# Kernel tuning notes

Hardware: AMD Instinct MI355X
Metric: run time of the kernel (lower is better)

## Reference

```python
import jax, jax.numpy as jnp
import numpy as np

B, T, D, L = 64, 512, 768, 5  # x batch is 2*B (MRC pairing), label_dim = L


def setup_inputs() -> dict:
    key = jax.random.key(0)
    k1, k2, k3, k4, k5 = jax.random.split(key, 5)
    x = jax.random.normal(k1, (2 * B, T, D), jnp.float32)
    label = jax.random.randint(k2, (B, T), 0, L - 1)            # values 0..L-2 so label+1 < L
    seqlen = jax.random.randint(k3, (B,), 2, T + 1)             # >=2 avoids degenerate CRF paths
    W = jax.random.normal(k4, (D, L), jnp.float32) * 0.02       # Dense kernel (TruncatedNormal 0.02)
    b = jnp.zeros((L,), jnp.float32)
    transitions = jax.random.normal(k5, (L, L), jnp.float32) * 0.1  # glorot-ish
    return {"x": x, "label": label, "seqlen": seqlen, "W": W, "b": b, "transitions": transitions}


def crf_log_norm(logits, seqlen, trans):
    # logits: [N, T, L]; forward algorithm with alphas frozen past seqlen
    ts = jnp.arange(1, logits.shape[1])

    def step(alpha, inp):
        x, t = inp  # x: [N, L]
        new = x + jax.nn.logsumexp(alpha[:, :, None] + trans[None], axis=1)
        return jnp.where((t < seqlen)[:, None], new, alpha), None

    alpha, _ = jax.lax.scan(step, logits[:, 0], (jnp.swapaxes(logits[:, 1:], 0, 1), ts))
    return jax.nn.logsumexp(alpha, axis=-1)


def crf_sequence_score(logits, tags, seqlen, trans):
    N, Tn, Ln = logits.shape
    t_idx = jnp.arange(Tn)
    mask = (t_idx[None, :] < seqlen[:, None]).astype(logits.dtype)          # [N, T]
    unary = jnp.take_along_axis(logits, tags[:, :, None], axis=2)[:, :, 0]  # [N, T]
    unary = jnp.sum(unary * mask, axis=1)
    binary = trans[tags[:, :-1], tags[:, 1:]]                               # [N, T-1]
    mask2 = (t_idx[None, 1:] < seqlen[:, None]).astype(logits.dtype)
    binary = jnp.sum(binary * mask2, axis=1)
    return unary + binary


def crf_decode(logits, trans, seqlen):
    # Viterbi: forward max + backpointers (identity past seqlen), then backtrack
    N, Tn, Ln = logits.shape
    ts = jnp.arange(1, Tn)
    ident = jnp.broadcast_to(jnp.arange(Ln)[None, :], (N, Ln))

    def fwd(state, inp):
        x, t = inp
        scores = state[:, :, None] + trans[None]   # [N, L_prev, L_cur]
        bp = jnp.argmax(scores, axis=1)            # [N, L]
        new = x + jnp.max(scores, axis=1)
        keep = (t < seqlen)[:, None]
        return jnp.where(keep, new, state), jnp.where(keep, bp, ident)

    last, bps = jax.lax.scan(fwd, logits[:, 0], (jnp.swapaxes(logits[:, 1:], 0, 1), ts))
    last_tag = jnp.argmax(last, axis=-1)           # [N]

    def bwd(tag, bp):
        prev = jnp.take_along_axis(bp, tag[:, None], axis=1)[:, 0]
        return prev, tag

    first_tag, rev_tags = jax.lax.scan(bwd, last_tag, bps, reverse=True)
    return jnp.concatenate([first_tag[:, None], jnp.swapaxes(rev_tags, 0, 1)], axis=1)  # [N, T]


def reference(x, label, seqlen, W, b, transitions):
    logits = x @ W + b                                   # [2B, T, L]
    label1 = jnp.where(label > 0, jnp.ones_like(label), label)
    label2 = jnp.where(label > 0, label + 1, label)
    label_r = jnp.concatenate([label1, label2], axis=0)  # [2B, T]
    seqlen_r = jnp.tile(seqlen, 2)                       # [2B]
    ll = crf_sequence_score(logits, label_r, seqlen_r, transitions) - crf_log_norm(logits, seqlen_r, transitions)
    loss = jnp.mean(-ll)
    vit = crf_decode(logits, transitions, seqlen_r)      # [2B, T]
    v1, v2 = jnp.split(vit, 2, axis=0)
    viterbi = jnp.where((v1 == 0) | (v2 == 0), jnp.zeros_like(v1), v2 - 1)
    mask = (jnp.arange(x.shape[1])[None, :] < seqlen[:, None]).astype(jnp.float32)
    acc = jnp.sum((viterbi == label).astype(jnp.float32) * mask) / jnp.sum(seqlen.astype(jnp.float32))
    return viterbi, loss, acc
```

## Files before the change

### kernel.cpp

```cpp
#include <hip/hip_runtime.h>

#define BB 64
#define TT 512
#define DD 768
#define LL 5
#define NSEQ 128
#define NTOK 65536
#define NEG_INF (-1e30f)
#define IDENT_W 0x4688u

__device__ __forceinline__ float wave_sum_dpp(float v) {
    int t;
    t = __builtin_amdgcn_update_dpp(0, __float_as_int(v), 0x111, 0xf, 0xf, false);
    v += __int_as_float(t);
    t = __builtin_amdgcn_update_dpp(0, __float_as_int(v), 0x112, 0xf, 0xf, false);
    v += __int_as_float(t);
    t = __builtin_amdgcn_update_dpp(0, __float_as_int(v), 0x114, 0xf, 0xf, false);
    v += __int_as_float(t);
    t = __builtin_amdgcn_update_dpp(0, __float_as_int(v), 0x118, 0xf, 0xf, false);
    v += __int_as_float(t);
    t = __builtin_amdgcn_update_dpp(0, __float_as_int(v), 0x142, 0xa, 0xf, false);
    v += __int_as_float(t);
    t = __builtin_amdgcn_update_dpp(0, __float_as_int(v), 0x143, 0xc, 0xf, false);
    v += __int_as_float(t);
    return v;
}

__global__ __launch_bounds__(256) void k_logits(const float* __restrict__ x,
                                                const float* __restrict__ W,
                                                const float* __restrict__ bias,
                                                const int* __restrict__ seqlen,
                                                float* __restrict__ logits) {
    const int lane = threadIdx.x & 63;
    const int w    = blockIdx.x * 4 + (threadIdx.x >> 6);
    const int n    = w & 127;
    const int slot = w >> 7;
    const int sl   = seqlen[n & (BB - 1)];
    if (slot >= sl) return;

    float wreg[3][4][LL];
    {
        const float4* W4 = reinterpret_cast<const float4*>(W);
#pragma unroll
        for (int p = 0; p < 3; ++p) {
            const int base4 = p * 320 + lane * 5;
#pragma unroll
            for (int j = 0; j < 5; ++j) {
                const float4 v = W4[base4 + j];
                wreg[p][(j * 4 + 0) / 5][(j * 4 + 0) % 5] = v.x;
                wreg[p][(j * 4 + 1) / 5][(j * 4 + 1) % 5] = v.y;
                wreg[p][(j * 4 + 2) / 5][(j * 4 + 2) % 5] = v.z;
                wreg[p][(j * 4 + 3) / 5][(j * 4 + 3) % 5] = v.w;
            }
        }
    }
    float breg[LL];
#pragma unroll
    for (int l = 0; l < LL; ++l) breg[l] = bias[l];

    const float* xb = x + (size_t)n * TT * DD;
    float* lb = logits + (size_t)n * TT * LL;

#pragma unroll
    for (int pp = 0; pp < 4; ++pp) {
        const int tA = slot + 128 * pp;
        if (tA >= sl) break;
        const int tB = tA + 64;
        const bool aB = (tB < sl);

        const float4* xpA = reinterpret_cast<const float4*>(xb + (size_t)tA * DD);
        const float4* xpB = reinterpret_cast<const float4*>(xb + (size_t)tB * DD);
        float4 vA[3], vB[3];
#pragma unroll
        for (int p = 0; p < 3; ++p) vA[p] = xpA[p * 64 + lane];
        if (aB) {
#pragma unroll
            for (int p = 0; p < 3; ++p) vB[p] = xpB[p * 64 + lane];
        }

        float accA[LL] = {0.f, 0.f, 0.f, 0.f, 0.f};
        float accB[LL] = {0.f, 0.f, 0.f, 0.f, 0.f};
#pragma unroll
        for (int p = 0; p < 3; ++p) {
#pragma unroll
            for (int l = 0; l < LL; ++l) {
                accA[l] += vA[p].x * wreg[p][0][l] + vA[p].y * wreg[p][1][l] +
                           vA[p].z * wreg[p][2][l] + vA[p].w * wreg[p][3][l];
            }
        }
        if (aB) {
#pragma unroll
            for (int p = 0; p < 3; ++p) {
#pragma unroll
                for (int l = 0; l < LL; ++l) {
                    accB[l] += vB[p].x * wreg[p][0][l] + vB[p].y * wreg[p][1][l] +
                               vB[p].z * wreg[p][2][l] + vB[p].w * wreg[p][3][l];
                }
            }
        }

#pragma unroll
        for (int l = 0; l < LL; ++l) accA[l] = wave_sum_dpp(accA[l]);
        if (aB) {
#pragma unroll
            for (int l = 0; l < LL; ++l) accB[l] = wave_sum_dpp(accB[l]);
        }

        if (lane == 63) {
#pragma unroll
            for (int l = 0; l < LL; ++l) lb[(size_t)tA * LL + l] = accA[l] + breg[l];
            if (aB) {
#pragma unroll
                for (int l = 0; l < LL; ++l) lb[(size_t)tB * LL + l] = accB[l] + breg[l];
            }
        }
    }
}

__global__ __launch_bounds__(512) void k_scan4(const float* __restrict__ logits,
                                               const int* __restrict__ label,
                                               const int* __restrict__ seqlen,
                                               const float* __restrict__ trans,
                                               float* __restrict__ out,
                                               float* __restrict__ losspart,
                                               int* __restrict__ okpart) {
    __shared__ float s_lg[2][TT * LL + 8];
    __shared__ float s_P[1600];
    __shared__ float s_Q[800];
    __shared__ float s_A[2][33 * 5];
    __shared__ float s_tr[25];
    __shared__ float s_etr[25];
    __shared__ unsigned s_mapw[2][32];
    __shared__ int s_B[2][33];
    __shared__ int s_tags[2][TT];
    __shared__ float s_ws[8];
    __shared__ int s_wok[8];

    const int tid = threadIdx.x;
    const int bid = blockIdx.x;

    if (bid < 128) {
        const int n  = bid;
        const int sl = seqlen[n & (BB - 1)];
        const float* lg = logits + (size_t)n * TT * LL;
        if (tid < 25) { const float tv = trans[tid]; s_tr[tid] = tv; s_etr[tid] = __expf(tv); }
        const int lim = sl * LL;
        for (int i = tid; i < lim; i += 512) s_lg[0][i] = lg[i];
        __syncthreads();

        {
            const bool sec = (n >= BB);
            const int* lab = label + (n & (BB - 1)) * TT;
            const int t = tid;
            float sc = 0.f;
            if (t < sl) {
                const int lv = lab[t];
                const int tg = (lv > 0) ? (sec ? lv + 1 : 1) : 0;
                sc = s_lg[0][t * 5 + tg];
                if (t >= 1) {
                    const int lp = lab[t - 1];
                    const int tp = (lp > 0) ? (sec ? lp + 1 : 1) : 0;
                    sc += s_tr[tp * 5 + tg];
                }
            }
#pragma unroll
            for (int off = 32; off > 0; off >>= 1) sc += __shfl_xor(sc, off, 64);
            if ((tid & 63) == 0) s_ws[tid >> 6] = sc;
        }

        if (tid < 320) {
            const int c = tid / 5, r = tid - 5 * c;
            float p[5];
#pragma unroll
            for (int j = 0; j < 5; ++j) p[j] = (j == r) ? 0.f : NEG_INF;
#pragma unroll
            for (int i = 0; i < 8; ++i) {
                const int t = c * 8 + 1 + i;
                const bool act = t < sl;
                const float m = fmaxf(fmaxf(fmaxf(p[0], p[1]), fmaxf(p[2], p[3])), p[4]);
                float e[5];
#pragma unroll
                for (int k = 0; k < 5; ++k) e[k] = __expf(p[k] - m);
                float nv[5];
#pragma unroll
                for (int j = 0; j < 5; ++j) {
                    float s = e[0] * s_etr[j];
#pragma unroll
                    for (int k = 1; k < 5; ++k) s += e[k] * s_etr[k * 5 + j];
                    nv[j] = m + __logf(s) + s_lg[0][t * 5 + j];
                }
#pragma unroll
                for (int j = 0; j < 5; ++j) p[j] = act ? nv[j] : p[j];
            }
#pragma unroll
            for (int j = 0; j < 5; ++j) s_P[c * 25 + r * 5 + j] = p[j];
        }
        __syncthreads();

#pragma unroll
        for (int lev = 0; lev < 6; ++lev) {
            const int np = 32 >> lev;
            const float* inb = (lev & 1) ? s_Q : s_P;
            float* outb      = (lev & 1) ? s_P : s_Q;
            for (int task = tid; task < np * 25; task += 512) {
                const int pm = task / 25;
                const int e  = task - pm * 25;
                const int r  = e / 5, j = e - 5 * r;
                const float* A  = inb + (2 * pm) * 25;
                const float* Bm = inb + (2 * pm + 1) * 25;
                float v[5];
#pragma unroll
                for (int k = 0; k < 5; ++k) v[k] = A[r * 5 + k] + Bm[k * 5 + j];
                float m = fmaxf(fmaxf(fmaxf(v[0], v[1]), fmaxf(v[2], v[3])), v[4]);
                float ssum = 0.f;
#pragma unroll
                for (int k = 0; k < 5; ++k) ssum += __expf(v[k] - m);
                outb[pm * 25 + e] = m + __logf(ssum);
            }
            __syncthreads();
        }

        if (tid == 0) {
            float b[5];
#pragma unroll
            for (int j = 0; j < 5; ++j) {
                float v[5];
#pragma unroll
                for (int k = 0; k < 5; ++k) v[k] = s_lg[0][k] + s_P[k * 5 + j];
                float m = fmaxf(fmaxf(fmaxf(v[0], v[1]), fmaxf(v[2], v[3])), v[4]);
                float ssum = 0.f;
#pragma unroll
                for (int k = 0; k < 5; ++k) ssum += __expf(v[k] - m);
                b[j] = m + __logf(ssum);
            }
            float m = fmaxf(fmaxf(fmaxf(b[0], b[1]), fmaxf(b[2], b[3])), b[4]);
            float ssum = 0.f;
#pragma unroll
            for (int j = 0; j < 5; ++j) ssum += __expf(b[j] - m);
            const float ln = m + __logf(ssum);
            float sc = 0.f;
#pragma unroll
            for (int wv = 0; wv < 8; ++wv) sc += s_ws[wv];
            losspart[n] = ln - sc;
        }
    } else {
        const int bb = bid - 128;
        const int sl = seqlen[bb];
        const float* lgA = logits + (size_t)bb * TT * LL;
        const float* lgB = logits + (size_t)(bb + BB) * TT * LL;

        if (tid < 25) s_tr[tid] = trans[tid];
        {
            const int lim = sl * LL;
            for (int i = tid; i < lim; i += 512) { s_lg[0][i] = lgA[i]; s_lg[1][i] = lgB[i]; }
        }
        __syncthreads();

        const int sid = tid / 160;
        const int rem = tid - sid * 160;
        const int cc  = rem / 5;
        const int rr  = rem - cc * 5;

        if (tid < 320) {
            float p[5];
#pragma unroll
            for (int j = 0; j < 5; ++j) p[j] = (j == rr) ? 0.f : NEG_INF;
#pragma unroll
            for (int i = 0; i < 16; ++i) {
                const int t = cc * 16 + 1 + i;
                const bool act = t < sl;
                float nv[5];
#pragma unroll
                for (int j = 0; j < 5; ++j) {
                    float b = p[0] + s_tr[j];
#pragma unroll
                    for (int k = 1; k < 5; ++k) b = fmaxf(b, p[k] + s_tr[k * 5 + j]);
                    nv[j] = b + s_lg[sid][t * 5 + j];
                }
#pragma unroll
                for (int j = 0; j < 5; ++j) p[j] = act ? nv[j] : p[j];
            }
#pragma unroll
            for (int j = 0; j < 5; ++j) s_P[sid * 800 + cc * 25 + rr * 5 + j] = p[j];
        }
        __syncthreads();

#pragma unroll
        for (int st = 1; st < 32; st <<= 1) {
            float Ar[5], Bm[25];
            const bool doit = (tid < 320) && (cc >= st);
            if (doit) {
#pragma unroll
                for (int k = 0; k < 5; ++k) Ar[k] = s_P[sid * 800 + (cc - st) * 25 + rr * 5 + k];
#pragma unroll
                for (int e = 0; e < 25; ++e) Bm[e] = s_P[sid * 800 + cc * 25 + e];
            }
            __syncthreads();
            if (doit) {
#pragma unroll
                for (int j = 0; j < 5; ++j) {
                    float b = Ar[0] + Bm[j];
#pragma unroll
                    for (int k = 1; k < 5; ++k) b = fmaxf(b, Ar[k] + Bm[k * 5 + j]);
                    s_P[sid * 800 + cc * 25 + rr * 5 + j] = b;
                }
            }
            __syncthreads();
        }

        if (tid < 320) {
            float b = s_lg[sid][0] + s_P[sid * 800 + cc * 25 + rr];
#pragma unroll
            for (int k = 1; k < 5; ++k)
                b = fmaxf(b, s_lg[sid][k] + s_P[sid * 800 + cc * 25 + k * 5 + rr]);
            s_A[sid][(cc + 1) * 5 + rr] = b;
        } else if (tid < 330) {
            const int i2 = tid - 320;
            const int s = i2 / 5, j = i2 - 5 * s;
            s_A[s][j] = s_lg[s][j];
        }
        __syncthreads();

        unsigned bpw[16];
        const int vs = tid >> 5, vc = tid & 31;
        if (tid < 64) {
            float a[5];
#pragma unroll
            for (int j = 0; j < 5; ++j) a[j] = s_A[vs][vc * 5 + j];
#pragma unroll
            for (int i = 0; i < 16; ++i) {
                const int t = vc * 16 + 1 + i;
                const bool act = t < sl;
                float nv[5]; int gi[5];
#pragma unroll
                for (int j = 0; j < 5; ++j) {
                    float b = a[0] + s_tr[j]; int g = 0;
#pragma unroll
                    for (int k = 1; k < 5; ++k) {
                        const float cn = a[k] + s_tr[k * 5 + j];
                        if (cn > b) { b = cn; g = k; }
                    }
                    nv[j] = b + s_lg[vs][t * 5 + j]; gi[j] = g;
                }
                const unsigned wv = (unsigned)gi[0] | ((unsigned)gi[1] << 3) |
                                    ((unsigned)gi[2] << 6) | ((unsigned)gi[3] << 9) |
                                    ((unsigned)gi[4] << 12);
                bpw[i] = act ? wv : IDENT_W;
#pragma unroll
                for (int j = 0; j < 5; ++j) a[j] = act ? nv[j] : a[j];
            }
            int m[5] = {0, 1, 2, 3, 4};
#pragma unroll
            for (int i = 15; i >= 0; --i) {
                const unsigned wv = bpw[i];
#pragma unroll
                for (int j = 0; j < 5; ++j) m[j] = (int)((wv >> (3 * m[j])) & 7u);
            }
            s_mapw[vs][vc] = (unsigned)m[0] | ((unsigned)m[1] << 3) | ((unsigned)m[2] << 6) |
                             ((unsigned)m[3] << 9) | ((unsigned)m[4] << 12);
        }
        __syncthreads();

        if (tid < 2) {
            const int s = tid;
            float b = s_A[s][32 * 5 + 0]; int lt = 0;
#pragma unroll
            for (int j = 1; j < 5; ++j) {
                const float cn = s_A[s][32 * 5 + j];
                if (cn > b) { b = cn; lt = j; }
            }
            unsigned wv[32];
#pragma unroll
            for (int c = 0; c < 32; ++c) wv[c] = s_mapw[s][c];
            int bc = lt; s_B[s][32] = lt;
#pragma unroll
            for (int c = 31; c >= 0; --c) { bc = (int)((wv[c] >> (3 * bc)) & 7u); s_B[s][c] = bc; }
        }
        __syncthreads();

        if (tid < 64) {
            int cur = s_B[vs][vc + 1];
#pragma unroll
            for (int i = 15; i >= 0; --i) {
                cur = (int)((bpw[i] >> (3 * cur)) & 7u);
                s_tags[vs][vc * 16 + i] = cur;
            }
        }
        __syncthreads();

        {
            const int t = tid;
            const int* lab = label + bb * TT;
            const int t1 = s_tags[0][t];
            const int t2 = s_tags[1][t];
            const int vit = (t1 == 0 || t2 == 0) ? 0 : (t2 - 1);
            out[bb * TT + t] = (float)vit;
            int ok = ((vit == lab[t]) && (t < sl)) ? 1 : 0;
#pragma unroll
            for (int off = 32; off > 0; off >>= 1) ok += __shfl_xor(ok, off, 64);
            if ((tid & 63) == 0) s_wok[tid >> 6] = ok;
        }
        __syncthreads();
        if (tid == 0) {
            int ok = 0;
#pragma unroll
            for (int wv = 0; wv < 8; ++wv) ok += s_wok[wv];
            okpart[bb] = ok;
        }
    }
}

__global__ __launch_bounds__(128) void k_final(const float* __restrict__ losspart,
                                               const int* __restrict__ okpart,
                                               const int* __restrict__ seqlen,
                                               float* __restrict__ out) {
    __shared__ float sf[2];
    __shared__ int s1[2], s2[2];
    const int tid = threadIdx.x;
    float f = losspart[tid];
    int ok = (tid < BB) ? okpart[tid] : 0;
    int sl = (tid < BB) ? seqlen[tid] : 0;
#pragma unroll
    for (int off = 32; off > 0; off >>= 1) {
        f  += __shfl_xor(f, off, 64);
        ok += __shfl_xor(ok, off, 64);
        sl += __shfl_xor(sl, off, 64);
    }
    if ((tid & 63) == 0) { sf[tid >> 6] = f; s1[tid >> 6] = ok; s2[tid >> 6] = sl; }
    __syncthreads();
    if (tid == 0) {
        out[BB * TT]     = (sf[0] + sf[1]) / (float)NSEQ;
        out[BB * TT + 1] = (float)(s1[0] + s1[1]) / (float)(s2[0] + s2[1]);
    }
}

extern "C" void kernel_launch(void* const* d_in, const int* in_sizes, int n_in,
                              void* d_out, int out_size, void* d_ws, size_t ws_size,
                              hipStream_t stream) {
    const float* x      = (const float*)d_in[0];
    const int*   label  = (const int*)d_in[1];
    const int*   seqlen = (const int*)d_in[2];
    const float* W      = (const float*)d_in[3];
    const float* bias   = (const float*)d_in[4];
    const float* trans  = (const float*)d_in[5];
    float* out = (float*)d_out;
    char*  ws  = (char*)d_ws;

    float* ws_logits   = (float*)(ws);
    float* ws_losspart = (float*)(ws + 1310720);
    int*   ws_okpart   = (int*)(ws + 1311232);

    hipLaunchKernelGGL(k_logits, dim3(2048), dim3(256), 0, stream,
                       x, W, bias, seqlen, ws_logits);
    hipLaunchKernelGGL(k_scan4, dim3(192), dim3(512), 0, stream,
                       ws_logits, label, seqlen, trans, out, ws_losspart, ws_okpart);
    hipLaunchKernelGGL(k_final, dim3(1), dim3(128), 0, stream,
                       ws_losspart, ws_okpart, seqlen, out);
}
```

Before: 39.55 us.

## Compact valid tokens via seqlen prefix sum for balanced logits GEMV

The logits kernel now builds a per-block prefix sum of sequence lengths and enumerates only valid tokens. Each wave takes tokens in a grid-stride loop and finds its sequence with a binary search. This replaces the fixed (sequence, slot) wave mapping, whose per-wave work was uneven across sequences of different lengths. In exchange, every block repeats the 128-element scan with several barriers, and each wave now processes one token per iteration instead of two, which reduces memory-level parallelism per wave.

```diff
diff --git a/kernel.cpp b/kernel.cpp
--- a/kernel.cpp
+++ b/kernel.cpp
@@ -31,12 +31,27 @@
                                                 const float* __restrict__ bias,
                                                 const int* __restrict__ seqlen,
                                                 float* __restrict__ logits) {
-    const int lane = threadIdx.x & 63;
-    const int w    = blockIdx.x * 4 + (threadIdx.x >> 6);
-    const int n    = w & 127;
-    const int slot = w >> 7;
-    const int sl   = seqlen[n & (BB - 1)];
-    if (slot >= sl) return;
+    __shared__ int sP[129];
+    __shared__ int tmp[128];
+    const int tid = threadIdx.x;
+
+    if (tid < 128) tmp[tid] = seqlen[tid & (BB - 1)];
+    __syncthreads();
+#pragma unroll
+    for (int off = 1; off < 128; off <<= 1) {
+        int v = 0;
+        if (tid < 128 && tid >= off) v = tmp[tid - off];
+        __syncthreads();
+        if (tid < 128) tmp[tid] += v;
+        __syncthreads();
+    }
+    if (tid < 128) sP[tid + 1] = tmp[tid];
+    if (tid == 0) sP[0] = 0;
+    __syncthreads();
+    const int A = sP[128];
+
+    const int lane = tid & 63;
+    const int wid  = blockIdx.x * 4 + (tid >> 6);
 
     float wreg[3][4][LL];
     {
@@ -58,61 +73,39 @@
 #pragma unroll
     for (int l = 0; l < LL; ++l) breg[l] = bias[l];
 
-    const float* xb = x + (size_t)n * TT * DD;
-    float* lb = logits + (size_t)n * TT * LL;
-
-#pragma unroll
-    for (int pp = 0; pp < 4; ++pp) {
-        const int tA = slot + 128 * pp;
-        if (tA >= sl) break;
-        const int tB = tA + 64;
-        const bool aB = (tB < sl);
-
-        const float4* xpA = reinterpret_cast<const float4*>(xb + (size_t)tA * DD);
-        const float4* xpB = reinterpret_cast<const float4*>(xb + (size_t)tB * DD);
-        float4 vA[3], vB[3];
-#pragma unroll
-        for (int p = 0; p < 3; ++p) vA[p] = xpA[p * 64 + lane];
-        if (aB) {
-#pragma unroll
-            for (int p = 0; p < 3; ++p) vB[p] = xpB[p * 64 + lane];
-        }
-
-        float accA[LL] = {0.f, 0.f, 0.f, 0.f, 0.f};
-        float accB[LL] = {0.f, 0.f, 0.f, 0.f, 0.f};
-#pragma unroll
-        for (int p = 0; p < 3; ++p) {
-#pragma unroll
-            for (int l = 0; l < LL; ++l) {
-                accA[l] += vA[p].x * wreg[p][0][l] + vA[p].y * wreg[p][1][l] +
-                           vA[p].z * wreg[p][2][l] + vA[p].w * wreg[p][3][l];
-            }
-        }
-        if (aB) {
-#pragma unroll
-            for (int p = 0; p < 3; ++p) {
-#pragma unroll
-                for (int l = 0; l < LL; ++l) {
-                    accB[l] += vB[p].x * wreg[p][0][l] + vB[p].y * wreg[p][1][l] +
-                               vB[p].z * wreg[p][2][l] + vB[p].w * wreg[p][3][l];
-                }
-            }
-        }
-
-#pragma unroll
-        for (int l = 0; l < LL; ++l) accA[l] = wave_sum_dpp(accA[l]);
-        if (aB) {
-#pragma unroll
-            for (int l = 0; l < LL; ++l) accB[l] = wave_sum_dpp(accB[l]);
-        }
+    for (int g = wid; g < A; g += 8192) {
+        int lo = 0, hi = 128;
+#pragma unroll
+        for (int s = 0; s < 7; ++s) {
+            const int mid = (lo + hi) >> 1;
+            if (sP[mid] <= g) lo = mid; else hi = mid;
+        }
+        const int n = lo;
+        const int t = g - sP[lo];
+        const size_t tok = (size_t)n * TT + t;
+
+        const float4* xp = reinterpret_cast<const float4*>(x + tok * DD);
+        float4 v0 = xp[lane];
+        float4 v1 = xp[64 + lane];
+        float4 v2 = xp[128 + lane];
+
+        float acc[LL];
+#pragma unroll
+        for (int l = 0; l < LL; ++l) {
+            acc[l] = v0.x * wreg[0][0][l] + v0.y * wreg[0][1][l] +
+                     v0.z * wreg[0][2][l] + v0.w * wreg[0][3][l] +
+                     v1.x * wreg[1][0][l] + v1.y * wreg[1][1][l] +
+                     v1.z * wreg[1][2][l] + v1.w * wreg[1][3][l] +
+                     v2.x * wreg[2][0][l] + v2.y * wreg[2][1][l] +
+                     v2.z * wreg[2][2][l] + v2.w * wreg[2][3][l];
+        }
+#pragma unroll
+        for (int l = 0; l < LL; ++l) acc[l] = wave_sum_dpp(acc[l]);
 
         if (lane == 63) {
 #pragma unroll
-            for (int l = 0; l < LL; ++l) lb[(size_t)tA * LL + l] = accA[l] + breg[l];
-            if (aB) {
-#pragma unroll
-                for (int l = 0; l < LL; ++l) lb[(size_t)tB * LL + l] = accB[l] + breg[l];
-            }
+            for (int l = 0; l < LL; ++l)
+                logits[tok * LL + l] = acc[l] + breg[l];
         }
     }
 }
```

Result: slower. 41.47 us (+4.9%).

## Fuse final reduction into scan kernel via last-block atomic counter; nontemporal x loads

Applied to the files above, without the earlier changes.

Removes the separate single-block k_final launch. Each k_scan4 block now bumps a global counter, and the last of the 192 blocks performs the loss and accuracy reduction. A hipMemsetAsync clears the counter before each launch. Separately, the streaming x reads in k_logits now use nontemporal loads through an ext_vector_type so they avoid polluting the cache. The change trades one kernel launch for a memset node plus atomics and fences, and depends on correct memory ordering between blocks.

```diff
diff --git a/kernel.cpp b/kernel.cpp
--- a/kernel.cpp
+++ b/kernel.cpp
@@ -8,6 +8,8 @@
 #define NTOK 65536
 #define NEG_INF (-1e30f)
 #define IDENT_W 0x4688u
+
+typedef float floatx4 __attribute__((ext_vector_type(4)));
 
 __device__ __forceinline__ float wave_sum_dpp(float v) {
     int t;
@@ -40,13 +42,13 @@
 
     float wreg[3][4][LL];
     {
-        const float4* W4 = reinterpret_cast<const float4*>(W);
+        const floatx4* W4 = reinterpret_cast<const floatx4*>(W);
 #pragma unroll
         for (int p = 0; p < 3; ++p) {
             const int base4 = p * 320 + lane * 5;
 #pragma unroll
             for (int j = 0; j < 5; ++j) {
-                const float4 v = W4[base4 + j];
+                const floatx4 v = W4[base4 + j];
                 wreg[p][(j * 4 + 0) / 5][(j * 4 + 0) % 5] = v.x;
                 wreg[p][(j * 4 + 1) / 5][(j * 4 + 1) % 5] = v.y;
                 wreg[p][(j * 4 + 2) / 5][(j * 4 + 2) % 5] = v.z;
@@ -68,14 +70,14 @@
         const int tB = tA + 64;
         const bool aB = (tB < sl);
 
-        const float4* xpA = reinterpret_cast<const float4*>(xb + (size_t)tA * DD);
-        const float4* xpB = reinterpret_cast<const float4*>(xb + (size_t)tB * DD);
-        float4 vA[3], vB[3];
-#pragma unroll
-        for (int p = 0; p < 3; ++p) vA[p] = xpA[p * 64 + lane];
+        const floatx4* xpA = reinterpret_cast<const floatx4*>(xb + (size_t)tA * DD);
+        const floatx4* xpB = reinterpret_cast<const floatx4*>(xb + (size_t)tB * DD);
+        floatx4 vA[3], vB[3];
+#pragma unroll
+        for (int p = 0; p < 3; ++p) vA[p] = __builtin_nontemporal_load(&xpA[p * 64 + lane]);
         if (aB) {
 #pragma unroll
-            for (int p = 0; p < 3; ++p) vB[p] = xpB[p * 64 + lane];
+            for (int p = 0; p < 3; ++p) vB[p] = __builtin_nontemporal_load(&xpB[p * 64 + lane]);
         }
 
         float accA[LL] = {0.f, 0.f, 0.f, 0.f, 0.f};
@@ -123,7 +125,8 @@
                                                const float* __restrict__ trans,
                                                float* __restrict__ out,
                                                float* __restrict__ losspart,
-                                               int* __restrict__ okpart) {
+                                               int* __restrict__ okpart,
+                                               int* __restrict__ ctr) {
     __shared__ float s_lg[2][TT * LL + 8];
     __shared__ float s_P[1600];
     __shared__ float s_Q[800];
@@ -135,6 +138,7 @@
     __shared__ int s_tags[2][TT];
     __shared__ float s_ws[8];
     __shared__ int s_wok[8];
+    __shared__ int s_last;
 
     const int tid = threadIdx.x;
     const int bid = blockIdx.x;
@@ -408,29 +412,29 @@
             okpart[bb] = ok;
         }
     }
-}
-
-__global__ __launch_bounds__(128) void k_final(const float* __restrict__ losspart,
-                                               const int* __restrict__ okpart,
-                                               const int* __restrict__ seqlen,
-                                               float* __restrict__ out) {
-    __shared__ float sf[2];
-    __shared__ int s1[2], s2[2];
-    const int tid = threadIdx.x;
-    float f = losspart[tid];
-    int ok = (tid < BB) ? okpart[tid] : 0;
-    int sl = (tid < BB) ? seqlen[tid] : 0;
-#pragma unroll
-    for (int off = 32; off > 0; off >>= 1) {
-        f  += __shfl_xor(f, off, 64);
-        ok += __shfl_xor(ok, off, 64);
-        sl += __shfl_xor(sl, off, 64);
-    }
-    if ((tid & 63) == 0) { sf[tid >> 6] = f; s1[tid >> 6] = ok; s2[tid >> 6] = sl; }
+
     __syncthreads();
     if (tid == 0) {
-        out[BB * TT]     = (sf[0] + sf[1]) / (float)NSEQ;
-        out[BB * TT + 1] = (float)(s1[0] + s1[1]) / (float)(s2[0] + s2[1]);
+        __threadfence();
+        s_last = (atomicAdd(ctr, 1) == 191) ? 1 : 0;
+    }
+    __syncthreads();
+    if (s_last && tid < 64) {
+        __threadfence();
+        float f = __hip_atomic_load(&losspart[tid], __ATOMIC_RELAXED, __HIP_MEMORY_SCOPE_AGENT) +
+                  __hip_atomic_load(&losspart[tid + 64], __ATOMIC_RELAXED, __HIP_MEMORY_SCOPE_AGENT);
+        int ok = __hip_atomic_load(&okpart[tid], __ATOMIC_RELAXED, __HIP_MEMORY_SCOPE_AGENT);
+        int sl = seqlen[tid];
+#pragma unroll
+        for (int off = 32; off > 0; off >>= 1) {
+            f  += __shfl_xor(f, off, 64);
+            ok += __shfl_xor(ok, off, 64);
+            sl += __shfl_xor(sl, off, 64);
+        }
+        if (tid == 0) {
+            out[BB * TT]     = f / (float)NSEQ;
+            out[BB * TT + 1] = (float)ok / (float)sl;
+        }
     }
 }
 
@@ -449,11 +453,12 @@
     float* ws_logits   = (float*)(ws);
     float* ws_losspart = (float*)(ws + 1310720);
     int*   ws_okpart   = (int*)(ws + 1311232);
-
+    int*   ws_ctr      = (int*)(ws + 1311488);
+
+    (void)hipMemsetAsync(ws_ctr, 0, 4, stream);
     hipLaunchKernelGGL(k_logits, dim3(2048), dim3(256), 0, stream,
                        x, W, bias, seqlen, ws_logits);
     hipLaunchKernelGGL(k_scan4, dim3(192), dim3(512), 0, stream,
-                       ws_logits, label, seqlen, trans, out, ws_losspart, ws_okpart);
-    hipLaunchKernelGGL(k_final, dim3(1), dim3(128), 0, stream,
-                       ws_losspart, ws_okpart, seqlen, out);
+                       ws_logits, label, seqlen, trans, out, ws_losspart,
+                       ws_okpart, ws_ctr);
 }
```

After: 49.62 us. 25.5% more time.
